# Performance work log

Measured on AMD Instinct MI355X. Metric: run time of the kernel, lower is better.

Reference implementation:

```python
import jax, jax.numpy as jnp
import numpy as np

HIDDEN = 1024
HEADS = 16
HEAD_DIM = HIDDEN // HEADS


def setup_inputs() -> dict:
    key = jax.random.key(0)
    ks = jax.random.split(key, 9)
    B, S = 2, 2048
    std = 0.02
    inp = {
        "query": jax.random.normal(ks[0], (B, S, HIDDEN), dtype=jnp.float32),
        "Wq": jax.random.normal(ks[1], (HIDDEN, HIDDEN), dtype=jnp.float32) * std,
        "bq": jnp.zeros((HIDDEN,), dtype=jnp.float32),
        "Wk": jax.random.normal(ks[2], (HIDDEN, HIDDEN), dtype=jnp.float32) * std,
        "bk": jnp.zeros((HIDDEN,), dtype=jnp.float32),
        "Wv": jax.random.normal(ks[3], (HIDDEN, HIDDEN), dtype=jnp.float32) * std,
        "bv": jnp.zeros((HIDDEN,), dtype=jnp.float32),
        "Wo": jax.random.normal(ks[4], (HIDDEN, HIDDEN), dtype=jnp.float32) * std,
        "bo": jnp.zeros((HIDDEN,), dtype=jnp.float32),
    }
    return inp


def reference(query, Wq, bq, Wk, bk, Wv, bv, Wo, bo):
    B, S, H = query.shape
    # torch nn.Linear: y = x @ W.T + b
    Q = query @ Wq.T + bq
    K = query @ Wk.T + bk  # key defaults to query (self-attention)
    V = query @ Wv.T + bv
    # [B, S, H] -> [B, heads, S, head_dim]
    def split_heads(x):
        return x.reshape(B, S, HEADS, HEAD_DIM).transpose(0, 2, 1, 3)
    Qh, Kh, Vh = split_heads(Q), split_heads(K), split_heads(V)
    scale = jnp.sqrt(jnp.asarray(HEAD_DIM, dtype=query.dtype))
    scores = jnp.einsum("bhqd,bhkd->bhqk", Qh, Kh) / scale
    attn = jax.nn.softmax(scores, axis=-1)  # dropout=0 (eval)
    context = jnp.einsum("bhqk,bhkd->bhqd", attn, Vh)
    context = context.transpose(0, 2, 1, 3).reshape(B, S, H)
    output = context @ Wo.T + bo
    return output, attn
```

## Files before the change

kernel.cpp:

```cpp
#include <hip/hip_runtime.h>
#include <hip/hip_bf16.h>
#include <cstdint>

typedef __attribute__((ext_vector_type(4))) float f32x4;
typedef __attribute__((ext_vector_type(8))) short bf16x8;

__device__ __forceinline__ unsigned short f2bf(float f){
  union { float f; unsigned int u; } v; v.f = f;
  unsigned int u = v.u;
  u += 0x7FFFu + ((u >> 16) & 1u);
  return (unsigned short)(u >> 16);
}
__device__ __forceinline__ float bf2f(unsigned short s){
  union { unsigned int u; float f; } v; v.u = ((unsigned int)s) << 16;
  return v.f;
}

__global__ __launch_bounds__(256) void cvt_bf16(const float* __restrict__ in,
                                                unsigned short* __restrict__ out,
                                                int n4){
  int i = blockIdx.x * 256 + threadIdx.x;
  if (i < n4){
    float4 v = ((const float4*)in)[i];
    ushort4 o;
    o.x = f2bf(v.x); o.y = f2bf(v.y); o.z = f2bf(v.z); o.w = f2bf(v.w);
    ((ushort4*)out)[i] = o;
  }
}

__global__ __launch_bounds__(256) void qkv_gemm(
    const unsigned short* __restrict__ A,
    const unsigned short* __restrict__ W0,
    const unsigned short* __restrict__ W1,
    const unsigned short* __restrict__ W2,
    const float* __restrict__ b0,
    const float* __restrict__ b1,
    const float* __restrict__ b2,
    unsigned short* __restrict__ Qo,
    unsigned short* __restrict__ Ko,
    unsigned short* __restrict__ Vto)
{
  __shared__ unsigned short As[2][128*64];
  __shared__ unsigned short Bs[2][128*64];

  const int K = 1024;
  const int tid = threadIdx.x;
  const int l   = tid & 63;
  const int wid = tid >> 6;
  const int g   = l >> 4;
  const int li  = l & 15;
  const int widx = blockIdx.x >> 3;
  const int m0  = blockIdx.y * 128;
  const int n0  = (blockIdx.x & 7) * 128;
  const int wm  = (wid >> 1) * 64;
  const int wn  = (wid & 1) * 64;
  const int srow = tid >> 3;
  const int sck  = tid & 7;

  const unsigned short* Bw = (widx == 0) ? W0 : ((widx == 1) ? W1 : W2);
  const float* bias        = (widx == 0) ? b0 : ((widx == 1) ? b1 : b2);

  const unsigned short* Ag = A  + (size_t)(m0 + srow) * K + sck * 8;
  const unsigned short* Bg = Bw + (size_t)(n0 + srow) * K + sck * 8;

  f32x4 acc[4][4] = {};
  bf16x8 ra[4], rb[4];
  const int NT = K >> 6;

  #pragma unroll
  for (int r = 0; r < 4; ++r){
    ra[r] = *(const bf16x8*)(Ag + (size_t)(r*32) * K);
    rb[r] = *(const bf16x8*)(Bg + (size_t)(r*32) * K);
  }
  #pragma unroll
  for (int r = 0; r < 4; ++r){
    const int row = srow + r*32;
    const int ck  = sck ^ (row & 7);
    *(bf16x8*)(&As[0][row*64 + ck*8]) = ra[r];
    *(bf16x8*)(&Bs[0][row*64 + ck*8]) = rb[r];
  }
  __syncthreads();

  int cur = 0;
  for (int kt = 0; kt < NT; ++kt){
    if (kt + 1 < NT){
      const int kof = (kt + 1) << 6;
      #pragma unroll
      for (int r = 0; r < 4; ++r){
        ra[r] = *(const bf16x8*)(Ag + (size_t)(r*32) * K + kof);
        rb[r] = *(const bf16x8*)(Bg + (size_t)(r*32) * K + kof);
      }
    }
    #pragma unroll
    for (int kk = 0; kk < 2; ++kk){
      bf16x8 af[4], bfr[4];
      #pragma unroll
      for (int f = 0; f < 4; ++f){
        const int rowa = wm + f*16 + li;
        const int cka  = (kk*4 + g) ^ (rowa & 7);
        af[f] = *(const bf16x8*)(&As[cur][rowa*64 + cka*8]);
        const int rowb = wn + f*16 + li;
        const int ckb  = (kk*4 + g) ^ (rowb & 7);
        bfr[f] = *(const bf16x8*)(&Bs[cur][rowb*64 + ckb*8]);
      }
      #pragma unroll
      for (int fm = 0; fm < 4; ++fm)
        #pragma unroll
        for (int fn = 0; fn < 4; ++fn)
          acc[fm][fn] = __builtin_amdgcn_mfma_f32_16x16x32_bf16(af[fm], bfr[fn], acc[fm][fn], 0, 0, 0);
    }
    __syncthreads();
    if (kt + 1 < NT){
      #pragma unroll
      for (int r = 0; r < 4; ++r){
        const int row = srow + r*32;
        const int ck  = sck ^ (row & 7);
        *(bf16x8*)(&As[cur^1][row*64 + ck*8]) = ra[r];
        *(bf16x8*)(&Bs[cur^1][row*64 + ck*8]) = rb[r];
      }
      __syncthreads();
    }
    cur ^= 1;
  }

  unsigned short* Oqk = (widx == 0) ? Qo : Ko;
  #pragma unroll
  for (int fn = 0; fn < 4; ++fn){
    const int col = n0 + wn + fn*16 + li;
    const float bv = bias[col];
    #pragma unroll
    for (int fm = 0; fm < 4; ++fm){
      #pragma unroll
      for (int j = 0; j < 4; ++j){
        const int row = m0 + wm + fm*16 + g*4 + j;
        const float v = acc[fm][fn][j] + bv;
        if (widx < 2){
          Oqk[(size_t)row * 1024 + col] = f2bf(v);
        } else {
          const int bb = row >> 11;
          const int s  = row & 2047;
          Vto[((size_t)(bb*1024 + col)) * 2048 + s] = f2bf(v);
        }
      }
    }
  }
}

__global__ __launch_bounds__(256) void gemm_bt(
    const unsigned short* __restrict__ A,
    const unsigned short* __restrict__ Bw,
    const float* __restrict__ bias,
    float* __restrict__ outp,
    int M, int N, int K)
{
  __shared__ unsigned short As[2][128*64];
  __shared__ unsigned short Bs[2][128*64];

  const int tid = threadIdx.x;
  const int l   = tid & 63;
  const int wid = tid >> 6;
  const int g   = l >> 4;
  const int li  = l & 15;
  const int m0  = blockIdx.y * 128;
  const int n0  = blockIdx.x * 128;
  const int wm  = (wid >> 1) * 64;
  const int wn  = (wid & 1) * 64;
  const int srow = tid >> 3;
  const int sck  = tid & 7;

  const unsigned short* Ag = A  + (size_t)(m0 + srow) * K + sck * 8;
  const unsigned short* Bg = Bw + (size_t)(n0 + srow) * K + sck * 8;

  f32x4 acc[4][4] = {};
  bf16x8 ra[4], rb[4];
  const int NT = K >> 6;

  #pragma unroll
  for (int r = 0; r < 4; ++r){
    ra[r] = *(const bf16x8*)(Ag + (size_t)(r*32) * K);
    rb[r] = *(const bf16x8*)(Bg + (size_t)(r*32) * K);
  }
  #pragma unroll
  for (int r = 0; r < 4; ++r){
    const int row = srow + r*32;
    const int ck  = sck ^ (row & 7);
    *(bf16x8*)(&As[0][row*64 + ck*8]) = ra[r];
    *(bf16x8*)(&Bs[0][row*64 + ck*8]) = rb[r];
  }
  __syncthreads();

  int cur = 0;
  for (int kt = 0; kt < NT; ++kt){
    if (kt + 1 < NT){
      const int kof = (kt + 1) << 6;
      #pragma unroll
      for (int r = 0; r < 4; ++r){
        ra[r] = *(const bf16x8*)(Ag + (size_t)(r*32) * K + kof);
        rb[r] = *(const bf16x8*)(Bg + (size_t)(r*32) * K + kof);
      }
    }
    #pragma unroll
    for (int kk = 0; kk < 2; ++kk){
      bf16x8 af[4], bfr[4];
      #pragma unroll
      for (int f = 0; f < 4; ++f){
        const int rowa = wm + f*16 + li;
        const int cka  = (kk*4 + g) ^ (rowa & 7);
        af[f] = *(const bf16x8*)(&As[cur][rowa*64 + cka*8]);
        const int rowb = wn + f*16 + li;
        const int ckb  = (kk*4 + g) ^ (rowb & 7);
        bfr[f] = *(const bf16x8*)(&Bs[cur][rowb*64 + ckb*8]);
      }
      #pragma unroll
      for (int fm = 0; fm < 4; ++fm)
        #pragma unroll
        for (int fn = 0; fn < 4; ++fn)
          acc[fm][fn] = __builtin_amdgcn_mfma_f32_16x16x32_bf16(af[fm], bfr[fn], acc[fm][fn], 0, 0, 0);
    }
    __syncthreads();
    if (kt + 1 < NT){
      #pragma unroll
      for (int r = 0; r < 4; ++r){
        const int row = srow + r*32;
        const int ck  = sck ^ (row & 7);
        *(bf16x8*)(&As[cur^1][row*64 + ck*8]) = ra[r];
        *(bf16x8*)(&Bs[cur^1][row*64 + ck*8]) = rb[r];
      }
      __syncthreads();
    }
    cur ^= 1;
  }

  #pragma unroll
  for (int fn = 0; fn < 4; ++fn){
    const int col = n0 + wn + fn*16 + li;
    const float bv = bias[col];
    #pragma unroll
    for (int fm = 0; fm < 4; ++fm){
      #pragma unroll
      for (int j = 0; j < 4; ++j){
        const int row = m0 + wm + fm*16 + g*4 + j;
        outp[(size_t)row * N + col] = acc[fm][fn][j] + bv;
      }
    }
  }
}

__global__ __launch_bounds__(512, 4) void attn_fused(
    const unsigned short* __restrict__ Qb,
    const unsigned short* __restrict__ Kb,
    const unsigned short* __restrict__ Vt,
    float* __restrict__ attn,
    unsigned short* __restrict__ ctxb)
{
  __shared__ float red[128];
  __shared__ __align__(16) unsigned short Pb[16 * 2048];
  float* ctxred = (float*)Pb;
  char*  Pbb    = (char*)Pb;

  const int tid = threadIdx.x;
  const int l   = tid & 63;
  const int w   = tid >> 6;
  const int g   = l >> 4;
  const int li  = l & 15;
  const int q0  = blockIdx.x * 16;
  const int bh  = blockIdx.y;
  const int b   = bh >> 4;
  const int h   = bh & 15;

  const size_t qrow = (size_t)(b*2048 + q0 + li) * 1024 + h*64 + g*8;
  const bf16x8 aq0 = *(const bf16x8*)(Qb + qrow);
  const bf16x8 aq1 = *(const bf16x8*)(Qb + qrow + 32);

  const unsigned short* Kbase = Kb + (size_t)(b*2048) * 1024 + h*64 + g*8;

  float ls = 0.f;
  const int swz = li << 3;
  #pragma unroll
  for (int hf = 0; hf < 2; ++hf){
    bf16x8 bk[16];
    #pragma unroll
    for (int cf = 0; cf < 8; ++cf){
      const unsigned short* kr = Kbase + (size_t)(w*256 + hf*128 + cf*16 + li) * 1024;
      bk[cf*2]   = *(const bf16x8*)(kr);
      bk[cf*2+1] = *(const bf16x8*)(kr + 32);
    }
    #pragma unroll
    for (int cf = 0; cf < 8; ++cf){
      f32x4 t = {};
      t = __builtin_amdgcn_mfma_f32_16x16x32_bf16(bk[cf*2],   aq0, t, 0, 0, 0);
      t = __builtin_amdgcn_mfma_f32_16x16x32_bf16(bk[cf*2+1], aq1, t, 0, 0, 0);
      const float p0 = __expf(t[0] * 0.125f);
      const float p1 = __expf(t[1] * 0.125f);
      const float p2 = __expf(t[2] * 0.125f);
      const float p3 = __expf(t[3] * 0.125f);
      ls += p0 + p1 + p2 + p3;
      ushort4 u;
      u.x = f2bf(p0); u.y = f2bf(p1); u.z = f2bf(p2); u.w = f2bf(p3);
      const int colb = w*512 + (hf*8 + cf)*32 + g*8;
      *(ushort4*)(Pbb + li*4096 + (colb ^ swz)) = u;
    }
  }

  ls += __shfl_xor(ls, 16);
  ls += __shfl_xor(ls, 32);
  if (l < 16) red[w*16 + l] = ls;
  __syncthreads();

  {
    #pragma unroll
    for (int rr = 0; rr < 2; ++rr){
      const int r = 2*w + rr;
      float dj = 0.f;
      #pragma unroll
      for (int ww = 0; ww < 8; ++ww) dj += red[ww*16 + r];
      const float rv = 1.0f / dj;
      const int key = r << 3;
      float* arow = attn + ((size_t)bh * 2048 + q0 + r) * 2048;
      #pragma unroll
      for (int c0 = 0; c0 < 8; ++c0){
        const int cb = c0*512 + l*8;
        const ushort4 u = *(const ushort4*)(Pbb + r*4096 + (cb ^ key));
        f32x4 o;
        o[0] = bf2f(u.x) * rv; o[1] = bf2f(u.y) * rv;
        o[2] = bf2f(u.z) * rv; o[3] = bf2f(u.w) * rv;
        *(f32x4*)(arow + c0*256 + l*4) = o;
      }
    }
  }

  f32x4 pv[4] = {};
  const unsigned short* Vbase = Vt + (size_t)(b*1024 + h*64) * 2048 + w*256;
  #pragma unroll
  for (int vh = 0; vh < 2; ++vh){
    bf16x8 vb[16];
    #pragma unroll
    for (int kt = 0; kt < 4; ++kt)
      #pragma unroll
      for (int df = 0; df < 4; ++df)
        vb[kt*4+df] = *(const bf16x8*)(Vbase + (size_t)(df*16 + li) * 2048 + (vh*4+kt)*32 + g*8);
    #pragma unroll
    for (int kt = 0; kt < 4; ++kt){
      const int colb2 = w*512 + (vh*4+kt)*64 + g*16;
      const ushort4 plo = *(const ushort4*)(Pbb + li*4096 + ( colb2      ^ swz));
      const ushort4 phi = *(const ushort4*)(Pbb + li*4096 + ((colb2 + 8) ^ swz));
      bf16x8 pa;
      pa[0] = plo.x; pa[1] = plo.y; pa[2] = plo.z; pa[3] = plo.w;
      pa[4] = phi.x; pa[5] = phi.y; pa[6] = phi.z; pa[7] = phi.w;
      #pragma unroll
      for (int df = 0; df < 4; ++df)
        pv[df] = __builtin_amdgcn_mfma_f32_16x16x32_bf16(pa, vb[kt*4+df], pv[df], 0, 0, 0);
    }
  }

  float r4[4];
  #pragma unroll
  for (int j = 0; j < 4; ++j){
    float dj = 0.f;
    #pragma unroll
    for (int ww = 0; ww < 8; ++ww) dj += red[ww*16 + g*4 + j];
    r4[j] = 1.0f / dj;
  }

  __syncthreads();
  #pragma unroll
  for (int df = 0; df < 4; ++df){
    #pragma unroll
    for (int j = 0; j < 4; ++j)
      ctxred[w*1024 + (g*4 + j)*64 + df*16 + li] = pv[df][j] * r4[j];
  }
  __syncthreads();
  {
    const int idx = tid * 2;
    const int r = idx >> 6;
    const int d = idx & 63;
    float v0 = 0.f, v1 = 0.f;
    #pragma unroll
    for (int ww = 0; ww < 8; ++ww){
      v0 += ctxred[ww*1024 + r*64 + d];
      v1 += ctxred[ww*1024 + r*64 + d + 1];
    }
    const unsigned int packed = (unsigned int)f2bf(v0) | ((unsigned int)f2bf(v1) << 16);
    *(unsigned int*)(ctxb + (size_t)(b*2048 + q0 + r) * 1024 + h*64 + d) = packed;
  }
}

extern "C" void kernel_launch(void* const* d_in, const int* in_sizes, int n_in,
                              void* d_out, int out_size, void* d_ws, size_t ws_size,
                              hipStream_t stream)
{
  const float* X  = (const float*)d_in[0];
  const float* Wq = (const float*)d_in[1];
  const float* bq = (const float*)d_in[2];
  const float* Wk = (const float*)d_in[3];
  const float* bk = (const float*)d_in[4];
  const float* Wv = (const float*)d_in[5];
  const float* bv = (const float*)d_in[6];
  const float* Wo = (const float*)d_in[7];
  const float* bo = (const float*)d_in[8];

  char* ws = (char*)d_ws;
  unsigned short* Xb  = (unsigned short*)(ws);
  unsigned short* Qb  = (unsigned short*)(ws + (size_t)( 8u<<20));
  unsigned short* Kbf = (unsigned short*)(ws + (size_t)(16u<<20));
  unsigned short* Vt  = (unsigned short*)(ws + (size_t)(24u<<20));
  unsigned short* Cb  = (unsigned short*)(ws + (size_t)(32u<<20));
  unsigned short* Wqb = (unsigned short*)(ws + (size_t)(40u<<20));
  unsigned short* Wkb = (unsigned short*)(ws + (size_t)(42u<<20));
  unsigned short* Wvb = (unsigned short*)(ws + (size_t)(44u<<20));
  unsigned short* Wob = (unsigned short*)(ws + (size_t)(46u<<20));

  float* out  = (float*)d_out;
  float* attn = out + (size_t)4194304;

  cvt_bf16<<<4096, 256, 0, stream>>>(X,  Xb,  1048576);
  cvt_bf16<<<1024, 256, 0, stream>>>(Wq, Wqb, 262144);
  cvt_bf16<<<1024, 256, 0, stream>>>(Wk, Wkb, 262144);
  cvt_bf16<<<1024, 256, 0, stream>>>(Wv, Wvb, 262144);
  cvt_bf16<<<1024, 256, 0, stream>>>(Wo, Wob, 262144);

  dim3 qkvgrid(24, 32);
  qkv_gemm<<<qkvgrid, 256, 0, stream>>>(Xb, Wqb, Wkb, Wvb, bq, bk, bv, Qb, Kbf, Vt);

  dim3 agrid(128, 32);
  attn_fused<<<agrid, 512, 0, stream>>>(Qb, Kbf, Vt, attn, Cb);

  dim3 ggrid(8, 32);
  gemm_bt<<<ggrid, 256, 0, stream>>>(Cb, Wob, bo, out, 4096, 1024, 1024);
}
```

Before: 382.2 us.

## Split attention-probability writeout into separate kernel that recomputes scores

The fused attention kernel no longer writes the full fp32 attention matrix. It now stores only the per-row reciprocal softmax denominators. A new attn_write kernel recomputes QK^T per tile, using K staged in shared memory, and writes normalized probabilities through a swizzled shared-memory buffer to get coalesced stores. K is also stored head-major by the QKV GEMM so K reads are contiguous. This trades recomputing the score matmul and exp for decoupling the large attention store from the context computation, and aims for better occupancy and write efficiency.

```diff
diff --git a/kernel.cpp b/kernel.cpp
--- a/kernel.cpp
+++ b/kernel.cpp
@@ -10,10 +10,6 @@
   unsigned int u = v.u;
   u += 0x7FFFu + ((u >> 16) & 1u);
   return (unsigned short)(u >> 16);
-}
-__device__ __forceinline__ float bf2f(unsigned short s){
-  union { unsigned int u; float f; } v; v.u = ((unsigned int)s) << 16;
-  return v.f;
 }
 
 __global__ __launch_bounds__(256) void cvt_bf16(const float* __restrict__ in,
@@ -37,7 +33,7 @@
     const float* __restrict__ b1,
     const float* __restrict__ b2,
     unsigned short* __restrict__ Qo,
-    unsigned short* __restrict__ Ko,
+    unsigned short* __restrict__ Khead,
     unsigned short* __restrict__ Vto)
 {
   __shared__ unsigned short As[2][128*64];
@@ -123,7 +119,6 @@
     cur ^= 1;
   }
 
-  unsigned short* Oqk = (widx == 0) ? Qo : Ko;
   #pragma unroll
   for (int fn = 0; fn < 4; ++fn){
     const int col = n0 + wn + fn*16 + li;
@@ -134,11 +129,14 @@
       for (int j = 0; j < 4; ++j){
         const int row = m0 + wm + fm*16 + g*4 + j;
         const float v = acc[fm][fn][j] + bv;
-        if (widx < 2){
-          Oqk[(size_t)row * 1024 + col] = f2bf(v);
+        const int bb = row >> 11;
+        const int s  = row & 2047;
+        if (widx == 0){
+          Qo[(size_t)row * 1024 + col] = f2bf(v);
+        } else if (widx == 1){
+          const int hh = col >> 6, dd = col & 63;
+          Khead[(((size_t)(bb*16 + hh))*2048 + s)*64 + dd] = f2bf(v);
         } else {
-          const int bb = row >> 11;
-          const int s  = row & 2047;
           Vto[((size_t)(bb*1024 + col)) * 2048 + s] = f2bf(v);
         }
       }
@@ -246,11 +244,11 @@
   }
 }
 
-__global__ __launch_bounds__(512, 4) void attn_fused(
+__global__ __launch_bounds__(512, 4) void attn_ctx(
     const unsigned short* __restrict__ Qb,
-    const unsigned short* __restrict__ Kb,
+    const unsigned short* __restrict__ Khead,
     const unsigned short* __restrict__ Vt,
-    float* __restrict__ attn,
+    float* __restrict__ rinv_g,
     unsigned short* __restrict__ ctxb)
 {
   __shared__ float red[128];
@@ -272,7 +270,7 @@
   const bf16x8 aq0 = *(const bf16x8*)(Qb + qrow);
   const bf16x8 aq1 = *(const bf16x8*)(Qb + qrow + 32);
 
-  const unsigned short* Kbase = Kb + (size_t)(b*2048) * 1024 + h*64 + g*8;
+  const unsigned short* Kbase = Khead + (size_t)bh * 2048 * 64 + g*8;
 
   float ls = 0.f;
   const int swz = li << 3;
@@ -281,7 +279,7 @@
     bf16x8 bk[16];
     #pragma unroll
     for (int cf = 0; cf < 8; ++cf){
-      const unsigned short* kr = Kbase + (size_t)(w*256 + hf*128 + cf*16 + li) * 1024;
+      const unsigned short* kr = Kbase + (size_t)(w*256 + hf*128 + cf*16 + li) * 64;
       bk[cf*2]   = *(const bf16x8*)(kr);
       bk[cf*2+1] = *(const bf16x8*)(kr + 32);
     }
@@ -307,26 +305,11 @@
   if (l < 16) red[w*16 + l] = ls;
   __syncthreads();
 
-  {
-    #pragma unroll
-    for (int rr = 0; rr < 2; ++rr){
-      const int r = 2*w + rr;
-      float dj = 0.f;
-      #pragma unroll
-      for (int ww = 0; ww < 8; ++ww) dj += red[ww*16 + r];
-      const float rv = 1.0f / dj;
-      const int key = r << 3;
-      float* arow = attn + ((size_t)bh * 2048 + q0 + r) * 2048;
-      #pragma unroll
-      for (int c0 = 0; c0 < 8; ++c0){
-        const int cb = c0*512 + l*8;
-        const ushort4 u = *(const ushort4*)(Pbb + r*4096 + (cb ^ key));
-        f32x4 o;
-        o[0] = bf2f(u.x) * rv; o[1] = bf2f(u.y) * rv;
-        o[2] = bf2f(u.z) * rv; o[3] = bf2f(u.w) * rv;
-        *(f32x4*)(arow + c0*256 + l*4) = o;
-      }
-    }
+  if (w == 0 && l < 16){
+    float ds = 0.f;
+    #pragma unroll
+    for (int ww = 0; ww < 8; ++ww) ds += red[ww*16 + l];
+    rinv_g[bh*2048 + q0 + l] = 1.0f / ds;
   }
 
   f32x4 pv[4] = {};
@@ -382,6 +365,78 @@
     }
     const unsigned int packed = (unsigned int)f2bf(v0) | ((unsigned int)f2bf(v1) << 16);
     *(unsigned int*)(ctxb + (size_t)(b*2048 + q0 + r) * 1024 + h*64 + d) = packed;
+  }
+}
+
+__global__ __launch_bounds__(256, 2) void attn_write(
+    const unsigned short* __restrict__ Qb,
+    const unsigned short* __restrict__ Khead,
+    const float* __restrict__ rinv_g,
+    float* __restrict__ attn)
+{
+  __shared__ unsigned short Ks[256*64];
+  __shared__ __align__(16) float Pw[4][16*128];
+  char* Kb8 = (char*)Ks;
+
+  const int tid = threadIdx.x;
+  const int l   = tid & 63;
+  const int w   = tid >> 6;
+  const int g   = l >> 4;
+  const int li  = l & 15;
+  const int kt  = blockIdx.x >> 5;
+  const int bh  = blockIdx.x & 31;
+  const int qt  = blockIdx.y;
+  const int b   = bh >> 4;
+  const int h   = bh & 15;
+
+  {
+    const unsigned short* Kg = Khead + ((size_t)bh * 2048 + kt*256) * 64;
+    #pragma unroll
+    for (int p = 0; p < 8; ++p){
+      const int key = p*32 + (tid >> 3);
+      const int c   = tid & 7;
+      const bf16x8 v = *(const bf16x8*)(Kg + (size_t)key * 64 + c*8);
+      *(bf16x8*)(Kb8 + key*128 + ((c ^ (key & 7)) * 16)) = v;
+    }
+  }
+  __syncthreads();
+
+  char* myPw = (char*)(&Pw[w][0]);
+
+  #pragma unroll
+  for (int rg = 0; rg < 2; ++rg){
+    const int qrow = qt*128 + w*32 + rg*16 + li;
+    const size_t qoff = (size_t)(b*2048 + qrow) * 1024 + h*64 + g*8;
+    const bf16x8 aq0 = *(const bf16x8*)(Qb + qoff);
+    const bf16x8 aq1 = *(const bf16x8*)(Qb + qoff + 32);
+    const float rv = rinv_g[bh*2048 + qrow];
+
+    #pragma unroll
+    for (int half = 0; half < 2; ++half){
+      #pragma unroll
+      for (int cf = 0; cf < 8; ++cf){
+        const int key = half*128 + cf*16 + li;
+        const bf16x8 k0 = *(const bf16x8*)(Kb8 + key*128 + (( g    ^ (key & 7)) * 16));
+        const bf16x8 k1 = *(const bf16x8*)(Kb8 + key*128 + (((g+4) ^ (key & 7)) * 16));
+        f32x4 t = {};
+        t = __builtin_amdgcn_mfma_f32_16x16x32_bf16(k0, aq0, t, 0, 0, 0);
+        t = __builtin_amdgcn_mfma_f32_16x16x32_bf16(k1, aq1, t, 0, 0, 0);
+        f32x4 p;
+        p[0] = __expf(t[0] * 0.125f) * rv;
+        p[1] = __expf(t[1] * 0.125f) * rv;
+        p[2] = __expf(t[2] * 0.125f) * rv;
+        p[3] = __expf(t[3] * 0.125f) * rv;
+        *(f32x4*)(myPw + li*512 + ((cf*64 + g*16) ^ ((li & 7) << 4))) = p;
+      }
+      const int lr = l & 31;
+      #pragma unroll
+      for (int i = 0; i < 8; ++i){
+        const int r = i*2 + (l >> 5);
+        const f32x4 v = *(const f32x4*)(myPw + r*512 + ((lr*16) ^ ((r & 7) << 4)));
+        const int qr = qt*128 + w*32 + rg*16 + r;
+        *(f32x4*)(attn + ((size_t)bh*2048 + qr)*2048 + kt*256 + half*128 + lr*4) = v;
+      }
+    }
   }
 }
 
@@ -400,15 +455,16 @@
   const float* bo = (const float*)d_in[8];
 
   char* ws = (char*)d_ws;
-  unsigned short* Xb  = (unsigned short*)(ws);
-  unsigned short* Qb  = (unsigned short*)(ws + (size_t)( 8u<<20));
-  unsigned short* Kbf = (unsigned short*)(ws + (size_t)(16u<<20));
-  unsigned short* Vt  = (unsigned short*)(ws + (size_t)(24u<<20));
-  unsigned short* Cb  = (unsigned short*)(ws + (size_t)(32u<<20));
-  unsigned short* Wqb = (unsigned short*)(ws + (size_t)(40u<<20));
-  unsigned short* Wkb = (unsigned short*)(ws + (size_t)(42u<<20));
-  unsigned short* Wvb = (unsigned short*)(ws + (size_t)(44u<<20));
-  unsigned short* Wob = (unsigned short*)(ws + (size_t)(46u<<20));
+  unsigned short* Xb    = (unsigned short*)(ws);
+  unsigned short* Qb    = (unsigned short*)(ws + (size_t)( 8u<<20));
+  unsigned short* Khead = (unsigned short*)(ws + (size_t)(16u<<20));
+  unsigned short* Vt    = (unsigned short*)(ws + (size_t)(24u<<20));
+  unsigned short* Cb    = (unsigned short*)(ws + (size_t)(32u<<20));
+  unsigned short* Wqb   = (unsigned short*)(ws + (size_t)(40u<<20));
+  unsigned short* Wkb   = (unsigned short*)(ws + (size_t)(42u<<20));
+  unsigned short* Wvb   = (unsigned short*)(ws + (size_t)(44u<<20));
+  unsigned short* Wob   = (unsigned short*)(ws + (size_t)(46u<<20));
+  float*          rinv  = (float*)(ws + (size_t)(48u<<20));
 
   float* out  = (float*)d_out;
   float* attn = out + (size_t)4194304;
@@ -420,10 +476,13 @@
   cvt_bf16<<<1024, 256, 0, stream>>>(Wo, Wob, 262144);
 
   dim3 qkvgrid(24, 32);
-  qkv_gemm<<<qkvgrid, 256, 0, stream>>>(Xb, Wqb, Wkb, Wvb, bq, bk, bv, Qb, Kbf, Vt);
+  qkv_gemm<<<qkvgrid, 256, 0, stream>>>(Xb, Wqb, Wkb, Wvb, bq, bk, bv, Qb, Khead, Vt);
 
   dim3 agrid(128, 32);
-  attn_fused<<<agrid, 512, 0, stream>>>(Qb, Kbf, Vt, attn, Cb);
+  attn_ctx<<<agrid, 512, 0, stream>>>(Qb, Khead, Vt, rinv, Cb);
+
+  dim3 wgrid(256, 16);
+  attn_write<<<wgrid, 256, 0, stream>>>(Qb, Khead, rinv, attn);
 
   dim3 ggrid(8, 32);
   gemm_bt<<<ggrid, 256, 0, stream>>>(Cb, Wob, bo, out, 4096, 1024, 1024);
```

Result: slower. 433.4 us (+13.4%).
